# Optimization experiments

Hardware: AMD Instinct MI355X
Metric: run time of the kernel (lower is better)

Reference implementation:

```python
import jax, jax.numpy as jnp
import numpy as np

# Keyed conv layer as structured SpMM in affine coordinates.
# W (N x N sparse, N = C*H*W + 1) stored in ELL format: for each output row r,
# cols[r, :] are the K column indices and vals[r, :] the nonzero values.
C, H, W_, KS = 32, 32, 32, 3
N = C * H * W_ + 1          # 32769, homogeneous (+1 bias) dim
K = C * KS * KS             # 288 nnz per row (Toeplitz conv structure)
B = 32                      # batch


def setup_inputs() -> dict:
    key = jax.random.key(0)
    k1, k2, k3 = jax.random.split(key, 3)
    x_affine = jax.random.normal(k1, (B, N), dtype=jnp.float32)
    cols = jax.random.randint(k2, (N, K), 0, N, dtype=jnp.int32)
    vals = jax.random.normal(k3, (N, K), dtype=jnp.float32) / np.float32(np.sqrt(K))
    return {"x_affine": x_affine, "vals": vals, "cols": cols}


def reference(x_affine, vals, cols):
    # y = (W @ x_affine^T)^T  with W in row-wise ELL format.
    # Gather input features addressed by each row's nonzero columns, then
    # contract over the K nonzeros of each row.
    xg = x_affine[:, cols]                      # [B, N, K] gathered features
    y = jnp.einsum('bnk,nk->bn', xg, vals)      # [B, N]
    return y
```

## Files before the change

### kernel.cpp

```cpp
#include <hip/hip_runtime.h>

constexpr int B = 32;
constexpr int N = 32 * 32 * 32 + 1;
constexpr int K = 32 * 3 * 3;

__global__ __launch_bounds__(256) void transpose_x_kernel(
    const float* __restrict__ x, float* __restrict__ xT) {
  __shared__ float tile[32][33];
  const int n0 = blockIdx.x * 32;
  const int t  = threadIdx.x;
  const int lb = t & 31;
  const int lr = t >> 5;
#pragma unroll
  for (int i = 0; i < 4; ++i) {
    const int b = lr + i * 8;
    const int n = n0 + lb;
    float v = 0.f;
    if (n < N) v = x[(size_t)b * N + n];
    tile[lb][b] = v;
  }
  __syncthreads();
#pragma unroll
  for (int i = 0; i < 4; ++i) {
    const int nl = lr + i * 8;
    const int n  = n0 + nl;
    if (n < N) xT[(size_t)n * B + lb] = tile[nl][lb];
  }
}

__global__ __launch_bounds__(256) void gather_dot_kernel(
    const float* __restrict__ xT, const float* __restrict__ vals,
    const int* __restrict__ cols, float* __restrict__ yT) {
  const int t    = threadIdx.x;
  const int lane = t & 63;
  const int wave = t >> 6;
  const int g    = lane >> 3;
  const int bq   = lane & 7;
  const int n    = blockIdx.x * 32 + wave * 8 + g;
  if (n >= N) return;

  const int*   __restrict__ crow = cols + (size_t)n * K;
  const float* __restrict__ vrow = vals + (size_t)n * K;

  float4 acc = make_float4(0.f, 0.f, 0.f, 0.f);

#pragma unroll 4
  for (int k = 0; k < K; k += 4) {
    const int4   c4 = *reinterpret_cast<const int4*>(crow + k);
    const float4 v4 = *reinterpret_cast<const float4*>(vrow + k);

    const float4 x0 = *reinterpret_cast<const float4*>(xT + (size_t)c4.x * B + bq * 4);
    const float4 x1 = *reinterpret_cast<const float4*>(xT + (size_t)c4.y * B + bq * 4);
    const float4 x2 = *reinterpret_cast<const float4*>(xT + (size_t)c4.z * B + bq * 4);
    const float4 x3 = *reinterpret_cast<const float4*>(xT + (size_t)c4.w * B + bq * 4);

    acc.x += x0.x * v4.x; acc.y += x0.y * v4.x; acc.z += x0.z * v4.x; acc.w += x0.w * v4.x;
    acc.x += x1.x * v4.y; acc.y += x1.y * v4.y; acc.z += x1.z * v4.y; acc.w += x1.w * v4.y;
    acc.x += x2.x * v4.z; acc.y += x2.y * v4.z; acc.z += x2.z * v4.z; acc.w += x2.w * v4.z;
    acc.x += x3.x * v4.w; acc.y += x3.y * v4.w; acc.z += x3.z * v4.w; acc.w += x3.w * v4.w;
  }

  *reinterpret_cast<float4*>(yT + (size_t)n * B + bq * 4) = acc;
}

__global__ __launch_bounds__(256) void transpose_y_kernel(
    const float* __restrict__ yT, float* __restrict__ y) {
  __shared__ float tile[32][33];
  const int n0 = blockIdx.x * 32;
  const int t  = threadIdx.x;
  const int lb = t & 31;
  const int lr = t >> 5;
#pragma unroll
  for (int i = 0; i < 4; ++i) {
    const int nl = lr + i * 8;
    const int n  = n0 + nl;
    float v = 0.f;
    if (n < N) v = yT[(size_t)n * B + lb];
    tile[nl][lb] = v;
  }
  __syncthreads();
#pragma unroll
  for (int i = 0; i < 4; ++i) {
    const int b = lr + i * 8;
    const int n = n0 + lb;
    if (n < N) y[(size_t)b * N + n] = tile[lb][b];
  }
}

__global__ __launch_bounds__(256) void gather_dot_fallback(
    const float* __restrict__ x, const float* __restrict__ vals,
    const int* __restrict__ cols, float* __restrict__ y) {
  const int t    = threadIdx.x;
  const int lane = t & 63;
  const int wave = t >> 6;
  const int g    = lane >> 3;
  const int bq   = lane & 7;
  const int n    = blockIdx.x * 32 + wave * 8 + g;
  if (n >= N) return;
  const int*   crow = cols + (size_t)n * K;
  const float* vrow = vals + (size_t)n * K;
  float4 acc = make_float4(0.f, 0.f, 0.f, 0.f);
  for (int k = 0; k < K; ++k) {
    const int   c = crow[k];
    const float v = vrow[k];
    acc.x += x[(size_t)(bq * 4 + 0) * N + c] * v;
    acc.y += x[(size_t)(bq * 4 + 1) * N + c] * v;
    acc.z += x[(size_t)(bq * 4 + 2) * N + c] * v;
    acc.w += x[(size_t)(bq * 4 + 3) * N + c] * v;
  }
  y[(size_t)(bq * 4 + 0) * N + n] = acc.x;
  y[(size_t)(bq * 4 + 1) * N + n] = acc.y;
  y[(size_t)(bq * 4 + 2) * N + n] = acc.z;
  y[(size_t)(bq * 4 + 3) * N + n] = acc.w;
}

extern "C" void kernel_launch(void* const* d_in, const int* in_sizes, int n_in,
                              void* d_out, int out_size, void* d_ws, size_t ws_size,
                              hipStream_t stream) {
  const float* x    = (const float*)d_in[0];
  const float* vals = (const float*)d_in[1];
  const int*   cols = (const int*)d_in[2];
  float*       y    = (float*)d_out;

  const size_t xT_elems = (size_t)N * B;
  const size_t need     = 2 * xT_elems * sizeof(float);

  const int nblocks = (N + 31) / 32;

  if (ws_size >= need) {
    float* xT = (float*)d_ws;
    float* yT = xT + xT_elems;
    transpose_x_kernel<<<nblocks, 256, 0, stream>>>(x, xT);
    gather_dot_kernel<<<nblocks, 256, 0, stream>>>(xT, vals, cols, yT);
    transpose_y_kernel<<<nblocks, 256, 0, stream>>>(yT, y);
  } else {
    gather_dot_fallback<<<nblocks, 256, 0, stream>>>(x, vals, cols, y);
  }
}
```

Before: 186.5 us.

## Split K reduction across two grid halves with dual accumulators and nontemporal loads

Splits the K=288 reduction of the gather-dot kernel into two halves across blockIdx.y, writing two partial yT buffers that the output transpose kernel sums. This doubles the number of blocks to raise parallelism and memory-level parallelism. Each thread also keeps two independent accumulators and uses nontemporal loads for the streamed cols and vals so they do not evict the reused xT data from cache. The cost is an extra N*B partial buffer, its write and read, and more workspace.

```diff
diff --git a/kernel.cpp b/kernel.cpp
--- a/kernel.cpp
+++ b/kernel.cpp
@@ -3,6 +3,10 @@
 constexpr int B = 32;
 constexpr int N = 32 * 32 * 32 + 1;
 constexpr int K = 32 * 3 * 3;
+constexpr int KHALF = K / 2;
+
+using i4 = __attribute__((ext_vector_type(4))) int;
+using f4 = __attribute__((ext_vector_type(4))) float;
 
 __global__ __launch_bounds__(256) void transpose_x_kernel(
     const float* __restrict__ x, float* __restrict__ xT) {
@@ -28,9 +32,10 @@
   }
 }
 
-__global__ __launch_bounds__(256) void gather_dot_kernel(
+__global__ __launch_bounds__(256) void gather_dot_ksplit_kernel(
     const float* __restrict__ xT, const float* __restrict__ vals,
-    const int* __restrict__ cols, float* __restrict__ yT) {
+    const int* __restrict__ cols, float* __restrict__ yT0,
+    float* __restrict__ yT1) {
   const int t    = threadIdx.x;
   const int lane = t & 63;
   const int wave = t >> 6;
@@ -39,32 +44,47 @@
   const int n    = blockIdx.x * 32 + wave * 8 + g;
   if (n >= N) return;
 
-  const int*   __restrict__ crow = cols + (size_t)n * K;
-  const float* __restrict__ vrow = vals + (size_t)n * K;
+  const int  k0   = blockIdx.y * KHALF;
+  const int* __restrict__ crow   = cols + (size_t)n * K + k0;
+  const float* __restrict__ vrow = vals + (size_t)n * K + k0;
 
-  float4 acc = make_float4(0.f, 0.f, 0.f, 0.f);
+  f4 acc0 = {0.f, 0.f, 0.f, 0.f};
+  f4 acc1 = {0.f, 0.f, 0.f, 0.f};
 
 #pragma unroll 4
-  for (int k = 0; k < K; k += 4) {
-    const int4   c4 = *reinterpret_cast<const int4*>(crow + k);
-    const float4 v4 = *reinterpret_cast<const float4*>(vrow + k);
+  for (int k = 0; k < KHALF; k += 8) {
+    const i4 cA = __builtin_nontemporal_load((const i4*)(crow + k));
+    const f4 vA = __builtin_nontemporal_load((const f4*)(vrow + k));
+    const i4 cB = __builtin_nontemporal_load((const i4*)(crow + k + 4));
+    const f4 vB = __builtin_nontemporal_load((const f4*)(vrow + k + 4));
 
-    const float4 x0 = *reinterpret_cast<const float4*>(xT + (size_t)c4.x * B + bq * 4);
-    const float4 x1 = *reinterpret_cast<const float4*>(xT + (size_t)c4.y * B + bq * 4);
-    const float4 x2 = *reinterpret_cast<const float4*>(xT + (size_t)c4.z * B + bq * 4);
-    const float4 x3 = *reinterpret_cast<const float4*>(xT + (size_t)c4.w * B + bq * 4);
+    const f4 xA0 = *reinterpret_cast<const f4*>(xT + (size_t)cA.x * B + bq * 4);
+    const f4 xA1 = *reinterpret_cast<const f4*>(xT + (size_t)cA.y * B + bq * 4);
+    const f4 xA2 = *reinterpret_cast<const f4*>(xT + (size_t)cA.z * B + bq * 4);
+    const f4 xA3 = *reinterpret_cast<const f4*>(xT + (size_t)cA.w * B + bq * 4);
+    const f4 xB0 = *reinterpret_cast<const f4*>(xT + (size_t)cB.x * B + bq * 4);
+    const f4 xB1 = *reinterpret_cast<const f4*>(xT + (size_t)cB.y * B + bq * 4);
+    const f4 xB2 = *reinterpret_cast<const f4*>(xT + (size_t)cB.z * B + bq * 4);
+    const f4 xB3 = *reinterpret_cast<const f4*>(xT + (size_t)cB.w * B + bq * 4);
 
-    acc.x += x0.x * v4.x; acc.y += x0.y * v4.x; acc.z += x0.z * v4.x; acc.w += x0.w * v4.x;
-    acc.x += x1.x * v4.y; acc.y += x1.y * v4.y; acc.z += x1.z * v4.y; acc.w += x1.w * v4.y;
-    acc.x += x2.x * v4.z; acc.y += x2.y * v4.z; acc.z += x2.z * v4.z; acc.w += x2.w * v4.z;
-    acc.x += x3.x * v4.w; acc.y += x3.y * v4.w; acc.z += x3.z * v4.w; acc.w += x3.w * v4.w;
+    acc0 += xA0 * vA.x;
+    acc0 += xA1 * vA.y;
+    acc0 += xA2 * vA.z;
+    acc0 += xA3 * vA.w;
+    acc1 += xB0 * vB.x;
+    acc1 += xB1 * vB.y;
+    acc1 += xB2 * vB.z;
+    acc1 += xB3 * vB.w;
   }
 
-  *reinterpret_cast<float4*>(yT + (size_t)n * B + bq * 4) = acc;
+  acc0 += acc1;
+  float* __restrict__ out = (blockIdx.y == 0) ? yT0 : yT1;
+  *reinterpret_cast<f4*>(out + (size_t)n * B + bq * 4) = acc0;
 }
 
-__global__ __launch_bounds__(256) void transpose_y_kernel(
-    const float* __restrict__ yT, float* __restrict__ y) {
+__global__ __launch_bounds__(256) void transpose_y_sum_kernel(
+    const float* __restrict__ yT0, const float* __restrict__ yT1,
+    float* __restrict__ y) {
   __shared__ float tile[32][33];
   const int n0 = blockIdx.x * 32;
   const int t  = threadIdx.x;
@@ -75,7 +95,10 @@
     const int nl = lr + i * 8;
     const int n  = n0 + nl;
     float v = 0.f;
-    if (n < N) v = yT[(size_t)n * B + lb];
+    if (n < N) {
+      const size_t idx = (size_t)n * B + lb;
+      v = yT0[idx] + yT1[idx];
+    }
     tile[nl][lb] = v;
   }
   __syncthreads();
@@ -122,17 +145,19 @@
   const int*   cols = (const int*)d_in[2];
   float*       y    = (float*)d_out;
 
-  const size_t xT_elems = (size_t)N * B;
-  const size_t need     = 2 * xT_elems * sizeof(float);
+  const size_t nb_elems = (size_t)N * B;
+  const size_t need     = 3 * nb_elems * sizeof(float);
 
   const int nblocks = (N + 31) / 32;
 
   if (ws_size >= need) {
-    float* xT = (float*)d_ws;
-    float* yT = xT + xT_elems;
+    float* xT  = (float*)d_ws;
+    float* yT0 = xT + nb_elems;
+    float* yT1 = yT0 + nb_elems;
     transpose_x_kernel<<<nblocks, 256, 0, stream>>>(x, xT);
-    gather_dot_kernel<<<nblocks, 256, 0, stream>>>(xT, vals, cols, yT);
-    transpose_y_kernel<<<nblocks, 256, 0, stream>>>(yT, y);
+    dim3 grid(nblocks, 2);
+    gather_dot_ksplit_kernel<<<grid, 256, 0, stream>>>(xT, vals, cols, yT0, yT1);
+    transpose_y_sum_kernel<<<nblocks, 256, 0, stream>>>(yT0, yT1, y);
   } else {
     gather_dot_fallback<<<nblocks, 256, 0, stream>>>(x, vals, cols, y);
   }
```

After: 216.8 us. 16.3% more time.

## Stage column indices in LDS via direct global-to-LDS loads and rotate k order

Applied to the files above, without the earlier changes.

Each block's 32 rows of column indices (36 KB) are copied into LDS with global_load_lds before any compute, so index reads come from shared memory instead of redundant per-lane global loads. The inner loop now handles 8 nonzeros per iteration with two accumulators, and each row-group starts at a rotated k offset to spread LDS bank and memory accesses. In exchange, the large LDS footprint lowers the number of blocks per CU, and the full staging step plus barrier adds latency before compute begins.

```diff
diff --git a/kernel.cpp b/kernel.cpp
--- a/kernel.cpp
+++ b/kernel.cpp
@@ -3,6 +3,9 @@
 constexpr int B = 32;
 constexpr int N = 32 * 32 * 32 + 1;
 constexpr int K = 32 * 3 * 3;
+
+using i4 = __attribute__((ext_vector_type(4))) int;
+using f4 = __attribute__((ext_vector_type(4))) float;
 
 __global__ __launch_bounds__(256) void transpose_x_kernel(
     const float* __restrict__ x, float* __restrict__ xT) {
@@ -28,39 +31,75 @@
   }
 }
 
-__global__ __launch_bounds__(256) void gather_dot_kernel(
+__global__ __launch_bounds__(256) void gather_dot_lds_kernel(
     const float* __restrict__ xT, const float* __restrict__ vals,
     const int* __restrict__ cols, float* __restrict__ yT) {
+  __shared__ int scols[32 * K];
   const int t    = threadIdx.x;
   const int lane = t & 63;
   const int wave = t >> 6;
   const int g    = lane >> 3;
   const int bq   = lane & 7;
-  const int n    = blockIdx.x * 32 + wave * 8 + g;
+  const int n0   = blockIdx.x * 32;
+
+  constexpr int SLAB_BYTES = 32 * K * 4;
+  constexpr int ROUNDS     = SLAB_BYTES / 4096;
+  const char* slab = (const char*)(cols + (size_t)n0 * K);
+  const long long avail = ((long long)N * K - (long long)n0 * K) * 4;
+#pragma unroll
+  for (int r = 0; r < ROUNDS; ++r) {
+    const int off  = r * 4096 + t * 16;
+    const int goff = (off + 16 <= avail) ? off : 0;
+    __builtin_amdgcn_global_load_lds(
+        (const __attribute__((address_space(1))) void*)(slab + goff),
+        (__attribute__((address_space(3))) void*)((char*)scols + off),
+        16, 0, 0);
+  }
+  __syncthreads();
+
+  const int nl = wave * 8 + g;
+  const int n  = n0 + nl;
   if (n >= N) return;
 
-  const int*   __restrict__ crow = cols + (size_t)n * K;
+  const int*   __restrict__ srow = scols + nl * K;
   const float* __restrict__ vrow = vals + (size_t)n * K;
 
-  float4 acc = make_float4(0.f, 0.f, 0.f, 0.f);
+  f4 acc0 = {0.f, 0.f, 0.f, 0.f};
+  f4 acc1 = {0.f, 0.f, 0.f, 0.f};
+
+  const int rot = g * 8;
 
 #pragma unroll 4
-  for (int k = 0; k < K; k += 4) {
-    const int4   c4 = *reinterpret_cast<const int4*>(crow + k);
-    const float4 v4 = *reinterpret_cast<const float4*>(vrow + k);
+  for (int k = 0; k < K; k += 8) {
+    int kk = k + rot;
+    if (kk >= K) kk -= K;
 
-    const float4 x0 = *reinterpret_cast<const float4*>(xT + (size_t)c4.x * B + bq * 4);
-    const float4 x1 = *reinterpret_cast<const float4*>(xT + (size_t)c4.y * B + bq * 4);
-    const float4 x2 = *reinterpret_cast<const float4*>(xT + (size_t)c4.z * B + bq * 4);
-    const float4 x3 = *reinterpret_cast<const float4*>(xT + (size_t)c4.w * B + bq * 4);
+    const i4 c0 = *reinterpret_cast<const i4*>(srow + kk);
+    const i4 c1 = *reinterpret_cast<const i4*>(srow + kk + 4);
+    const f4 v0 = *reinterpret_cast<const f4*>(vrow + kk);
+    const f4 v1 = *reinterpret_cast<const f4*>(vrow + kk + 4);
 
-    acc.x += x0.x * v4.x; acc.y += x0.y * v4.x; acc.z += x0.z * v4.x; acc.w += x0.w * v4.x;
-    acc.x += x1.x * v4.y; acc.y += x1.y * v4.y; acc.z += x1.z * v4.y; acc.w += x1.w * v4.y;
-    acc.x += x2.x * v4.z; acc.y += x2.y * v4.z; acc.z += x2.z * v4.z; acc.w += x2.w * v4.z;
-    acc.x += x3.x * v4.w; acc.y += x3.y * v4.w; acc.z += x3.z * v4.w; acc.w += x3.w * v4.w;
+    const f4 x0 = *reinterpret_cast<const f4*>(xT + (size_t)c0.x * B + bq * 4);
+    const f4 x1 = *reinterpret_cast<const f4*>(xT + (size_t)c0.y * B + bq * 4);
+    const f4 x2 = *reinterpret_cast<const f4*>(xT + (size_t)c0.z * B + bq * 4);
+    const f4 x3 = *reinterpret_cast<const f4*>(xT + (size_t)c0.w * B + bq * 4);
+    const f4 x4 = *reinterpret_cast<const f4*>(xT + (size_t)c1.x * B + bq * 4);
+    const f4 x5 = *reinterpret_cast<const f4*>(xT + (size_t)c1.y * B + bq * 4);
+    const f4 x6 = *reinterpret_cast<const f4*>(xT + (size_t)c1.z * B + bq * 4);
+    const f4 x7 = *reinterpret_cast<const f4*>(xT + (size_t)c1.w * B + bq * 4);
+
+    acc0 += x0 * v0.x;
+    acc0 += x1 * v0.y;
+    acc0 += x2 * v0.z;
+    acc0 += x3 * v0.w;
+    acc1 += x4 * v1.x;
+    acc1 += x5 * v1.y;
+    acc1 += x6 * v1.z;
+    acc1 += x7 * v1.w;
   }
 
-  *reinterpret_cast<float4*>(yT + (size_t)n * B + bq * 4) = acc;
+  acc0 += acc1;
+  *reinterpret_cast<f4*>(yT + (size_t)n * B + bq * 4) = acc0;
 }
 
 __global__ __launch_bounds__(256) void transpose_y_kernel(
@@ -122,16 +161,16 @@
   const int*   cols = (const int*)d_in[2];
   float*       y    = (float*)d_out;
 
-  const size_t xT_elems = (size_t)N * B;
-  const size_t need     = 2 * xT_elems * sizeof(float);
+  const size_t nb_elems = (size_t)N * B;
+  const size_t need     = 2 * nb_elems * sizeof(float);
 
   const int nblocks = (N + 31) / 32;
 
   if (ws_size >= need) {
     float* xT = (float*)d_ws;
-    float* yT = xT + xT_elems;
+    float* yT = xT + nb_elems;
     transpose_x_kernel<<<nblocks, 256, 0, stream>>>(x, xT);
-    gather_dot_kernel<<<nblocks, 256, 0, stream>>>(xT, vals, cols, yT);
+    gather_dot_lds_kernel<<<nblocks, 256, 0, stream>>>(xT, vals, cols, yT);
     transpose_y_kernel<<<nblocks, 256, 0, stream>>>(yT, y);
   } else {
     gather_dot_fallback<<<nblocks, 256, 0, stream>>>(x, vals, cols, y);
```

Result: faster. 176.2 us (-5.5%).
